# Kernel optimization log

Hardware: AMD Instinct MI355X
Metric: run time of the kernel (lower is better)

The kernel has to match this reference:

```python
import jax, jax.numpy as jnp
import numpy as np

B, C, H, W = 2, 512, 64, 64
S = 2            # scale_factor
HEADS = 8
GROUPS = 32      # assumed GroupNorm groups for group_norm(in_channels)
DK = C // HEADS
SCALE = 1.0 / DK ** 2   # faithful to source: 1/d_k**2
RES = H // S
R = RES * 2 - 1


def setup_inputs() -> dict:
    key = jax.random.key(0)
    ks = jax.random.split(key, 8)
    f = lambda k, shp, s=0.02: jax.random.normal(k, shp, jnp.float32) * s
    return {
        "x": jax.random.normal(ks[0], (B, C, H, W), jnp.float32),
        "q_w": f(ks[1], (C, C, 1, 1)),
        "q_b": jnp.zeros((C,), jnp.float32),
        "kv_w": f(ks[2], (2 * C, C, 1, 1)),
        "kv_b": jnp.zeros((2 * C,), jnp.float32),
        "off1_w": f(ks[3], (C, C, S, S)),
        "off1_b": jnp.zeros((C,), jnp.float32),
        "gn_w": jnp.ones((C,), jnp.float32),
        "gn_b": jnp.zeros((C,), jnp.float32),
        "off2_w": f(ks[4], (2, C, 1, 1)),
        "rpe_table": f(ks[5], (HEADS, R, R), 0.01),
        "proj_w": f(ks[6], (C, C, 1, 1)),
        "proj_b": jnp.zeros((C,), jnp.float32),
    }


def _conv(x, w, b=None, stride=1):
    y = jax.lax.conv_general_dilated(x, w, (stride, stride), 'VALID',
                                     dimension_numbers=('NCHW', 'OIHW', 'NCHW'))
    return y if b is None else y + b[None, :, None, None]


def _group_norm(x, w, b, eps=1e-5):
    n, c, h, wd = x.shape
    xg = x.reshape(n, GROUPS, -1)
    mu = xg.mean(-1, keepdims=True)
    var = xg.var(-1, keepdims=True)
    xg = (xg - mu) * jax.lax.rsqrt(var + eps)
    return xg.reshape(n, c, h, wd) * w[None, :, None, None] + b[None, :, None, None]


def _grid_sample(img, grid):
    # bilinear, align_corners=True; img [B,C,H,W], grid [B,...,2] in (x,y) order
    Bn, Cn, Hn, Wn = img.shape
    gshape = grid.shape[1:-1]
    g = grid.reshape(Bn, -1, 2)
    x = (g[..., 0] + 1.0) * 0.5 * (Wn - 1)
    y = (g[..., 1] + 1.0) * 0.5 * (Hn - 1)
    x0 = jnp.floor(x); y0 = jnp.floor(y)
    wx = (x - x0)[:, None, :]; wy = (y - y0)[:, None, :]
    x0i = jnp.clip(x0.astype(jnp.int32), 0, Wn - 1)
    x1i = jnp.clip(x0i + 1, 0, Wn - 1)
    y0i = jnp.clip(y0.astype(jnp.int32), 0, Hn - 1)
    y1i = jnp.clip(y0i + 1, 0, Hn - 1)
    imf = img.reshape(Bn, Cn, Hn * Wn)
    gat = lambda yi, xi: jnp.take_along_axis(imf, (yi * Wn + xi)[:, None, :], axis=2)
    out = (gat(y0i, x0i) * (1 - wx) * (1 - wy) + gat(y0i, x1i) * wx * (1 - wy)
           + gat(y1i, x0i) * (1 - wx) * wy + gat(y1i, x1i) * wx * wy)
    return out.reshape(Bn, Cn, *gshape)


def _forward(x, q_w, q_b, kv_w, kv_b, off1_w, off1_b, gn_w, gn_b, off2_w,
             rpe_table, proj_w, proj_b):
    l = H * W
    q = _conv(x, q_w, q_b)                                   # [B,C,H,W]
    t = _conv(q, off1_w, off1_b, stride=S)                   # [B,C,h,w]
    t = jax.nn.gelu(_group_norm(t, gn_w, gn_b), approximate=False)
    offset = _conv(t, off2_w).transpose(0, 2, 3, 1)          # [B,h,w,2] (y,x)
    h, w = offset.shape[1], offset.shape[2]
    n = h * w
    # reference points (linspace 0.5..h-0.5, normalized by h-1)
    ry = (jnp.linspace(0.5, h - 0.5, h) / (h - 1.0)) * 2.0 - 1.0
    rx = (jnp.linspace(0.5, w - 0.5, w) / (w - 1.0)) * 2.0 - 1.0
    ref = jnp.stack(jnp.meshgrid(ry, rx, indexing='ij'), -1)  # [h,w,2]
    pos = jnp.clip(offset + ref[None], -1.0, 1.0)             # [B,h,w,2]
    sampled = _grid_sample(x, pos[..., ::-1])                 # [B,C,h,w] (context=x)
    kv = _conv(sampled.reshape(B, C, 1, n), kv_w, kv_b)       # [B,2C,1,n]
    k, v = kv[:, :C], kv[:, C:]
    qf = q.reshape(B * HEADS, DK, l)
    kf = k.reshape(B * HEADS, DK, n)
    vf = v.reshape(B * HEADS, DK, n)
    attn = jnp.einsum('bcm,bcn->bmn', qf, kf) * SCALE         # [B*H, l, n]
    # query grid (arange, normalized by dim-1)
    gy = jnp.arange(H, dtype=jnp.float32) / (H - 1.0) * 2.0 - 1.0
    gx = jnp.arange(W, dtype=jnp.float32) / (W - 1.0) * 2.0 - 1.0
    qg = jnp.stack(jnp.meshgrid(gy, gx, indexing='ij'), -1).reshape(l, 2)
    disp = (qg[None, :, None, :] - pos.reshape(B, 1, n, 2)) * 0.5  # [B,l,n,2]
    rpe = jnp.broadcast_to(rpe_table[None], (B, HEADS, R, R))
    bias = _grid_sample(rpe, disp[..., ::-1])                  # [B,HEADS,l,n]
    attn = jax.nn.softmax(attn + bias.reshape(B * HEADS, l, n), axis=-1)
    out = jnp.einsum('bmn,bcn->bcm', attn, vf).reshape(B, C, H, W)
    return _conv(out, proj_w, proj_b)


def reference(x, q_w, q_b, kv_w, kv_b, off1_w, off1_b, gn_w, gn_b, off2_w,
              rpe_table, proj_w, proj_b):
    return _forward(x, q_w, q_b, kv_w, kv_b, off1_w, off1_b, gn_w, gn_b,
                    off2_w, rpe_table, proj_w, proj_b)
```

## Files before the change

### kernel.cpp

```cpp
#include <hip/hip_runtime.h>
#include <hip/hip_bf16.h>
#include <math.h>

typedef float floatx4 __attribute__((ext_vector_type(4)));
typedef short shortx8 __attribute__((ext_vector_type(8)));
typedef unsigned short ush;

#define NB    2
#define NC    512
#define NL    4096
#define NN    1024
#define NH    8
#define NDK   64
#define NR    63
#define LOG2E 1.44269504f
#define QT_SCALE (1.44269504f/4096.0f)

#define OFF_Q      0u
#define OFF_AO     0u
#define OFF_SMP    2097152u
#define OFF_QT     4194304u
#define OFF_T      6291456u
#define OFF_GS     7340032u
#define OFF_POS    7340160u
#define OFF_KT     7344256u
#define OFF_VV     7868544u
#define OFF_PART   8392832u
#define OFF_TAB4   8392832u

__device__ __forceinline__ ush f2bf(float f) {
    unsigned u = __float_as_uint(f);
    u += 0x7fffu + ((u >> 16) & 1u);
    return (ush)(u >> 16);
}
__device__ __forceinline__ float bf2f(ush h) {
    return __uint_as_float(((unsigned)h) << 16);
}

template<int NP, int BSRC, int OUTMODE>
__global__ __launch_bounds__(256) void gemm_mfma_k(
    const float* __restrict__ A, const void* __restrict__ Bv,
    const float* __restrict__ bias, void* __restrict__ Yv, void* __restrict__ Y2,
    int M, int K, int P, int KS)
{
    __shared__ ush a_hi[128 * 72];
    __shared__ ush b_hi[64 * 72];
    __shared__ ush a_lo[NP == 3 ? 128 * 72 : 64];
    __shared__ ush b_lo[NP == 3 ? 64 * 72 : 64];

    int tid = threadIdx.x;
    int wv = tid >> 6, lane = tid & 63, quad = lane >> 4, l15 = lane & 15;
    int bz = blockIdx.z;
    int b = bz / KS, ks = bz - b * KS;
    int m0 = blockIdx.y * 128, p0 = blockIdx.x * 64;
    int Ksl = K / KS, kbeg = ks * Ksl;

    floatx4 acc[2][4];
    #pragma unroll
    for (int mt = 0; mt < 2; ++mt)
        #pragma unroll
        for (int pt = 0; pt < 4; ++pt) acc[mt][pt] = (floatx4)0.f;

    for (int kc = 0; kc < Ksl; kc += 64) {
        int kg0 = kbeg + kc;
        #pragma unroll
        for (int r = 0; r < 8; ++r) {
            int idx = r * 256 + tid;
            int m = idx >> 4, k4 = (idx & 15) << 2;
            float4 av = *(const float4*)(A + (size_t)(m0 + m) * K + kg0 + k4);
            int o = m * 72 + k4;
            ush h0 = f2bf(av.x), h1 = f2bf(av.y), h2 = f2bf(av.z), h3 = f2bf(av.w);
            a_hi[o] = h0; a_hi[o + 1] = h1; a_hi[o + 2] = h2; a_hi[o + 3] = h3;
            if (NP == 3) {
                a_lo[o]     = f2bf(av.x - bf2f(h0));
                a_lo[o + 1] = f2bf(av.y - bf2f(h1));
                a_lo[o + 2] = f2bf(av.z - bf2f(h2));
                a_lo[o + 3] = f2bf(av.w - bf2f(h3));
            }
        }
        #pragma unroll
        for (int r = 0; r < 8; ++r) {
            int idx = r * 256 + tid;
            int k = idx >> 5, p2 = (idx & 31) << 1;
            float v0, v1;
            if (BSRC == 0) {
                const float* Bp = (const float*)Bv + (size_t)b * K * P;
                float2 t2 = *(const float2*)(Bp + (size_t)(kg0 + k) * P + p0 + p2);
                v0 = t2.x; v1 = t2.y;
            } else if (BSRC == 1) {
                const float* Bp = (const float*)Bv + (size_t)b * NC * NL;
                int kk = kg0 + k;
                int c = kk >> 2, kh = (kk >> 1) & 1, kw = kk & 1;
                int p = p0 + p2;
                int oh = p >> 5, ow = p & 31;
                const float* base = Bp + (size_t)c * NL + (2 * oh + kh) * 64 + kw;
                v0 = base[2 * ow];
                v1 = base[2 * ow + 2];
            } else {
                const ush* Bp = (const ush*)Bv + (size_t)b * K * P;
                unsigned u = *(const unsigned*)(Bp + (size_t)(kg0 + k) * P + p0 + p2);
                v0 = bf2f((ush)(u & 0xffffu));
                v1 = bf2f((ush)(u >> 16));
            }
            ush h0 = f2bf(v0), h1 = f2bf(v1);
            b_hi[p2 * 72 + k] = h0;
            b_hi[(p2 + 1) * 72 + k] = h1;
            if (NP == 3) {
                b_lo[p2 * 72 + k]       = f2bf(v0 - bf2f(h0));
                b_lo[(p2 + 1) * 72 + k] = f2bf(v1 - bf2f(h1));
            }
        }
        __syncthreads();

        shortx8 ah[2][2], al[2][2];
        #pragma unroll
        for (int mt = 0; mt < 2; ++mt)
            #pragma unroll
            for (int kk = 0; kk < 2; ++kk) {
                int o = (wv * 32 + mt * 16 + l15) * 72 + kk * 32 + quad * 8;
                ah[mt][kk] = *(const shortx8*)&a_hi[o];
                if (NP == 3) al[mt][kk] = *(const shortx8*)&a_lo[o];
            }
        #pragma unroll
        for (int pt = 0; pt < 4; ++pt) {
            #pragma unroll
            for (int kk = 0; kk < 2; ++kk) {
                int o = (pt * 16 + l15) * 72 + kk * 32 + quad * 8;
                shortx8 bh = *(const shortx8*)&b_hi[o];
                acc[0][pt] = __builtin_amdgcn_mfma_f32_16x16x32_bf16(ah[0][kk], bh, acc[0][pt], 0, 0, 0);
                acc[1][pt] = __builtin_amdgcn_mfma_f32_16x16x32_bf16(ah[1][kk], bh, acc[1][pt], 0, 0, 0);
                if (NP == 3) {
                    shortx8 bl = *(const shortx8*)&b_lo[o];
                    acc[0][pt] = __builtin_amdgcn_mfma_f32_16x16x32_bf16(ah[0][kk], bl, acc[0][pt], 0, 0, 0);
                    acc[1][pt] = __builtin_amdgcn_mfma_f32_16x16x32_bf16(ah[1][kk], bl, acc[1][pt], 0, 0, 0);
                    acc[0][pt] = __builtin_amdgcn_mfma_f32_16x16x32_bf16(al[0][kk], bh, acc[0][pt], 0, 0, 0);
                    acc[1][pt] = __builtin_amdgcn_mfma_f32_16x16x32_bf16(al[1][kk], bh, acc[1][pt], 0, 0, 0);
                }
            }
        }
        __syncthreads();
    }

    #pragma unroll
    for (int mt = 0; mt < 2; ++mt) {
        #pragma unroll
        for (int reg = 0; reg < 4; ++reg) {
            int m = m0 + wv * 32 + mt * 16 + quad * 4 + reg;
            float bb = (OUTMODE == 2) ? 0.f : bias[m];
            #pragma unroll
            for (int pt = 0; pt < 4; ++pt) {
                int p = p0 + pt * 16 + l15;
                float val = acc[mt][pt][reg] + bb;
                if (OUTMODE == 0) {
                    ((float*)Yv)[(size_t)b * M * P + (size_t)m * P + p] = val;
                } else if (OUTMODE == 2) {
                    ((float*)Yv)[(size_t)(ks * NB + b) * M * P + (size_t)m * P + p] = val;
                } else if (OUTMODE == 3) {
                    ((float*)Yv)[(size_t)b * M * P + (size_t)m * P + p] = val;
                    int h = m >> 6, d = m & 63;
                    ((ush*)Y2)[(((size_t)(b * 8 + h) * 4096) + p) * 64 + d] = f2bf(val * QT_SCALE);
                } else {
                    if (m < 512) {
                        int h = m >> 6, d = m & 63;
                        ((ush*)Yv)[(((size_t)(b * 8 + h) * 1024) + p) * 64 + d] = f2bf(val);
                    } else {
                        int c = m - 512;
                        ((ush*)Y2)[((size_t)(b * 512) + c) * 1024 + p] = f2bf(val);
                    }
                }
            }
        }
    }
}

__global__ __launch_bounds__(256) void reduce_off1_k(const float* __restrict__ part,
                                                     const float* __restrict__ bias,
                                                     float* __restrict__ t)
{
    int i = blockIdx.x * 256 + threadIdx.x;
    float v = part[i] + part[i + 1048576] + part[i + 2097152] + part[i + 3145728];
    t[i] = v + bias[(i >> 10) & 511];
}

__global__ __launch_bounds__(256) void gn_stats_k(const float* __restrict__ T, float* __restrict__ gs)
{
    int bg = blockIdx.x;
    const float* base = T + (size_t)bg * 16384;
    float s = 0.f, ss = 0.f;
    for (int i = threadIdx.x; i < 16384; i += 256) { float v = base[i]; s += v; ss += v * v; }
    #pragma unroll
    for (int off = 32; off >= 1; off >>= 1) { s += __shfl_xor(s, off); ss += __shfl_xor(ss, off); }
    __shared__ float red[8];
    int wv = threadIdx.x >> 6;
    if ((threadIdx.x & 63) == 0) { red[wv * 2] = s; red[wv * 2 + 1] = ss; }
    __syncthreads();
    if (threadIdx.x == 0) {
        float S = red[0] + red[2] + red[4] + red[6];
        float SS = red[1] + red[3] + red[5] + red[7];
        float mu = S / 16384.f;
        float var = SS / 16384.f - mu * mu;
        gs[bg * 2] = mu;
        gs[bg * 2 + 1] = rsqrtf(var + 1e-5f);
    }
}

__global__ __launch_bounds__(256) void gn_gelu_k(float* __restrict__ T, const float* __restrict__ gs,
                                                 const float* __restrict__ gw, const float* __restrict__ gb)
{
    int idx = blockIdx.x * 256 + threadIdx.x;
    int bg = idx >> 14;
    int c = (idx >> 10) & 511;
    float mu = gs[bg * 2], rs = gs[bg * 2 + 1];
    float v = (T[idx] - mu) * rs * gw[c] + gb[c];
    T[idx] = v * 0.5f * (1.f + erff(v * 0.70710678118654752f));
}

__global__ __launch_bounds__(256) void offset_pos_k(const float* __restrict__ T,
                                                    const float* __restrict__ w2,
                                                    float* __restrict__ pos)
{
    int b = blockIdx.x >> 5;
    int og = threadIdx.x & 31;
    int cg = threadIdx.x >> 5;
    int op = ((blockIdx.x & 31) << 5) + og;
    const float* Tb = T + (size_t)b * NC * NN + (size_t)cg * 64 * NN + op;
    float o0 = 0.f, o1 = 0.f;
    #pragma unroll 4
    for (int c = 0; c < 64; ++c) {
        float tv = Tb[(size_t)c * NN];
        o0 += w2[cg * 64 + c] * tv;
        o1 += w2[512 + cg * 64 + c] * tv;
    }
    __shared__ float rs[2][8][32];
    rs[0][cg][og] = o0;
    rs[1][cg][og] = o1;
    __syncthreads();
    if (threadIdx.x < 64) {
        int coord = threadIdx.x >> 5, og2 = threadIdx.x & 31;
        float s = 0.f;
        #pragma unroll
        for (int k = 0; k < 8; ++k) s += rs[coord][k][og2];
        int opf = ((blockIdx.x & 31) << 5) + og2;
        int oh = opf >> 5, ow = opf & 31;
        float ref = (coord == 0) ? ((0.5f + oh) / 31.f * 2.f - 1.f)
                                 : ((0.5f + ow) / 31.f * 2.f - 1.f);
        pos[((size_t)b * 1024 + opf) * 2 + coord] = fminf(fmaxf(s + ref, -1.f), 1.f);
    }
}

__global__ __launch_bounds__(256) void sample_k(const float* __restrict__ x,
                                                const float* __restrict__ pos,
                                                ush* __restrict__ smp)
{
    int idx = blockIdx.x * 256 + threadIdx.x;
    int j = idx & 1023, c = (idx >> 10) & 511, b = idx >> 19;
    float py = pos[(b * 1024 + j) * 2];
    float px = pos[(b * 1024 + j) * 2 + 1];
    float fx = (px + 1.f) * 0.5f * 63.f;
    float fy = (py + 1.f) * 0.5f * 63.f;
    float flx = floorf(fx), fly = floorf(fy);
    float wx = fx - flx, wy = fy - fly;
    int x0 = min(max((int)flx, 0), 63), y0 = min(max((int)fly, 0), 63);
    int x1 = min(x0 + 1, 63),           y1 = min(y0 + 1, 63);
    const float* xb = x + ((size_t)(b * NC + c)) * NL;
    float v00 = xb[y0 * 64 + x0];
    float v01 = xb[y0 * 64 + x1];
    float v10 = xb[y1 * 64 + x0];
    float v11 = xb[y1 * 64 + x1];
    float v = v00 * (1 - wx) * (1 - wy) + v01 * wx * (1 - wy)
            + v10 * (1 - wx) * wy       + v11 * wx * wy;
    smp[idx] = f2bf(v);
}

__global__ __launch_bounds__(256) void tab4_k(const float* __restrict__ rpe,
                                              uint2* __restrict__ tab4)
{
    int i = blockIdx.x * 256 + threadIdx.x;
    int h = i >> 12, y = (i >> 6) & 63, x = i & 63;
    const float* R = rpe + (size_t)h * 3969;
    float v00 = (y < 63 && x < 63)         ? R[y * 63 + x] * LOG2E : 0.f;
    float v01 = (y < 63 && x + 1 < 63)     ? R[y * 63 + x + 1] * LOG2E : 0.f;
    float v10 = (y + 1 < 63 && x < 63)     ? R[(y + 1) * 63 + x] * LOG2E : 0.f;
    float v11 = (y + 1 < 63 && x + 1 < 63) ? R[(y + 1) * 63 + x + 1] * LOG2E : 0.f;
    uint2 o;
    o.x = (unsigned)f2bf(v00) | ((unsigned)f2bf(v01) << 16);
    o.y = (unsigned)f2bf(v10) | ((unsigned)f2bf(v11) << 16);
    tab4[i] = o;
}

__global__ __launch_bounds__(256) void attn_k(
    const ush* __restrict__ qT, const ush* __restrict__ kT,
    const ush* __restrict__ vv, const float* __restrict__ pos,
    const uint2* __restrict__ tab4, ush* __restrict__ ao)
{
    __shared__ __align__(16) char smem[50176];
    ush*   pa     = (ush*)smem;
    uint2* tab_s  = (uint2*)(smem + 9216);
    float* posj15 = (float*)(smem + 41984);
    float* obuf   = (float*)smem;

    int bh = blockIdx.y;
    int b = bh >> 3, h = bh & 7;
    int m0 = blockIdx.x * 64;
    int tid = threadIdx.x;
    int wv = tid >> 6, lane = tid & 63, quad = lane >> 4, l15 = lane & 15;

    const ush* qbase = qT + ((size_t)bh * 4096 + m0 + wv * 16 + l15) * 64 + quad * 8;
    shortx8 qf0 = *(const shortx8*)(qbase);
    shortx8 qf1 = *(const shortx8*)(qbase + 32);

    const uint2* tg = tab4 + (size_t)h * 4096;
    for (int i = tid; i < 4096; i += 256) tab_s[i] = tg[i];
    const float* pb = pos + (size_t)b * 2048;
    for (int i = tid; i < 2048; i += 256) posj15[i] = pb[i] * 15.5f;

    float qy15[4], qx15[4];
    #pragma unroll
    for (int reg = 0; reg < 4; ++reg) {
        int mg = m0 + wv * 16 + quad * 4 + reg;
        qy15[reg] = (float)(mg >> 6) * (31.f / 63.f) + 15.5f;
        qx15[reg] = (float)(mg & 63) * (31.f / 63.f) + 15.5f;
    }

    floatx4 o_acc[4], o_sum;
    #pragma unroll
    for (int dt = 0; dt < 4; ++dt) o_acc[dt] = (floatx4)0.f;
    o_sum = (floatx4)0.f;
    shortx8 vone = {16256, 16256, 16256, 16256, 16256, 16256, 16256, 16256};

    __syncthreads();

    const ush* kbase = kT + (size_t)bh * 1024 * 64;
    const ush* vbase = vv + (size_t)(b * 512 + h * 64) * 1024;

    for (int jc = 0; jc < 16; ++jc) {
        int j0 = jc * 64;
        floatx4 sacc[4];
        #pragma unroll
        for (int jt = 0; jt < 4; ++jt) sacc[jt] = (floatx4)0.f;
        #pragma unroll
        for (int jt = 0; jt < 4; ++jt) {
            const ush* kp = kbase + (size_t)(j0 + jt * 16 + l15) * 64 + quad * 8;
            shortx8 kf0 = *(const shortx8*)kp;
            shortx8 kf1 = *(const shortx8*)(kp + 32);
            sacc[jt] = __builtin_amdgcn_mfma_f32_16x16x32_bf16(qf0, kf0, sacc[jt], 0, 0, 0);
            sacc[jt] = __builtin_amdgcn_mfma_f32_16x16x32_bf16(qf1, kf1, sacc[jt], 0, 0, 0);
        }
        #pragma unroll
        for (int jt = 0; jt < 4; ++jt) {
            int j = j0 + jt * 16 + l15;
            float2 pp = *(const float2*)&posj15[j * 2];
            #pragma unroll
            for (int reg = 0; reg < 4; ++reg) {
                float gy = qy15[reg] - pp.x;
                float gx = qx15[reg] - pp.y;
                float fy = floorf(gy), fx = floorf(gx);
                float wy = gy - fy, wx = gx - fx;
                int y0 = min(max((int)fy, 0), 62);
                int x0 = min(max((int)fx, 0), 62);
                uint2 tw = tab_s[(y0 << 6) + x0];
                float r00 = __uint_as_float(tw.x << 16);
                float r01 = __uint_as_float(tw.x & 0xffff0000u);
                float r10 = __uint_as_float(tw.y << 16);
                float r11 = __uint_as_float(tw.y & 0xffff0000u);
                float bx0 = r00 + wx * (r01 - r00);
                float bx1 = r10 + wx * (r11 - r10);
                float p = exp2f(sacc[jt][reg] + (bx0 + wy * (bx1 - bx0)));
                pa[(wv * 16 + quad * 4 + reg) * 72 + jt * 16 + l15] = f2bf(p);
            }
        }
        const ush* pbase = pa + (wv * 16 + l15) * 72 + quad * 8;
        shortx8 pf0 = *(const shortx8*)pbase;
        shortx8 pf1 = *(const shortx8*)(pbase + 32);
        o_sum = __builtin_amdgcn_mfma_f32_16x16x32_bf16(pf0, vone, o_sum, 0, 0, 0);
        o_sum = __builtin_amdgcn_mfma_f32_16x16x32_bf16(pf1, vone, o_sum, 0, 0, 0);
        #pragma unroll
        for (int dt = 0; dt < 4; ++dt) {
            const ush* vp = vbase + (size_t)(dt * 16 + l15) * 1024 + j0 + quad * 8;
            shortx8 vf0 = *(const shortx8*)vp;
            shortx8 vf1 = *(const shortx8*)(vp + 32);
            o_acc[dt] = __builtin_amdgcn_mfma_f32_16x16x32_bf16(pf0, vf0, o_acc[dt], 0, 0, 0);
            o_acc[dt] = __builtin_amdgcn_mfma_f32_16x16x32_bf16(pf1, vf1, o_acc[dt], 0, 0, 0);
        }
    }

    __syncthreads();
    float inv[4];
    #pragma unroll
    for (int reg = 0; reg < 4; ++reg) inv[reg] = 1.f / o_sum[reg];
    #pragma unroll
    for (int dt = 0; dt < 4; ++dt)
        #pragma unroll
        for (int reg = 0; reg < 4; ++reg)
            obuf[(dt * 16 + l15) * 68 + wv * 16 + quad * 4 + reg] = o_acc[dt][reg] * inv[reg];
    __syncthreads();
    ush* aobase = ao + ((size_t)(b * 512 + h * 64)) * 4096 + m0;
    for (int i = tid; i < 4096; i += 256) {
        int d = i >> 6, m = i & 63;
        aobase[(size_t)d * 4096 + m] = f2bf(obuf[d * 68 + m]);
    }
}

extern "C" void kernel_launch(void* const* d_in, const int* in_sizes, int n_in,
                              void* d_out, int out_size, void* d_ws, size_t ws_size,
                              hipStream_t stream) {
    const float* x      = (const float*)d_in[0];
    const float* q_w    = (const float*)d_in[1];
    const float* q_b    = (const float*)d_in[2];
    const float* kv_w   = (const float*)d_in[3];
    const float* kv_b   = (const float*)d_in[4];
    const float* off1_w = (const float*)d_in[5];
    const float* off1_b = (const float*)d_in[6];
    const float* gn_w   = (const float*)d_in[7];
    const float* gn_b   = (const float*)d_in[8];
    const float* off2_w = (const float*)d_in[9];
    const float* rpe    = (const float*)d_in[10];
    const float* proj_w = (const float*)d_in[11];
    const float* proj_b = (const float*)d_in[12];

    float* ws   = (float*)d_ws;
    float* q    = ws + OFF_Q;
    ush*   ao   = (ush*)(ws + OFF_AO);
    ush*   smp  = (ush*)(ws + OFF_SMP);
    ush*   qT   = (ush*)(ws + OFF_QT);
    float* t    = ws + OFF_T;
    float* gs   = ws + OFF_GS;
    float* pos  = ws + OFF_POS;
    ush*   kT   = (ush*)(ws + OFF_KT);
    ush*   vv   = (ush*)(ws + OFF_VV);
    float* part = ws + OFF_PART;
    uint2* tab4 = (uint2*)(ws + OFF_TAB4);
    float* out  = (float*)d_out;

    gemm_mfma_k<3, 0, 3><<<dim3(64, 4, 2), 256, 0, stream>>>(q_w, x, q_b, q, qT, 512, 512, 4096, 1);
    gemm_mfma_k<3, 1, 2><<<dim3(16, 4, 8), 256, 0, stream>>>(off1_w, q, nullptr, part, nullptr, 512, 2048, 1024, 4);
    reduce_off1_k<<<4096, 256, 0, stream>>>(part, off1_b, t);
    gn_stats_k<<<64, 256, 0, stream>>>(t, gs);
    gn_gelu_k<<<4096, 256, 0, stream>>>(t, gs, gn_w, gn_b);
    offset_pos_k<<<64, 256, 0, stream>>>(t, off2_w, pos);
    tab4_k<<<128, 256, 0, stream>>>(rpe, tab4);
    sample_k<<<4096, 256, 0, stream>>>(x, pos, smp);
    gemm_mfma_k<1, 2, 4><<<dim3(16, 8, 2), 256, 0, stream>>>(kv_w, smp, kv_b, kT, vv, 1024, 512, 1024, 1);
    attn_k<<<dim3(64, 16), 256, 0, stream>>>(qT, kT, vv, pos, tab4, ao);
    gemm_mfma_k<1, 2, 0><<<dim3(64, 4, 2), 256, 0, stream>>>(proj_w, ao, proj_b, out, nullptr, 512, 512, 4096, 1);
}
```

Measured before the change: 368.6 us.

## Fold q conv into offset conv weights and enlarge attention blocks

```diff
diff --git a/kernel.cpp b/kernel.cpp
--- a/kernel.cpp
+++ b/kernel.cpp
@@ -16,17 +16,18 @@
 #define LOG2E 1.44269504f
 #define QT_SCALE (1.44269504f/4096.0f)
 
-#define OFF_Q      0u
-#define OFF_AO     0u
-#define OFF_SMP    2097152u
-#define OFF_QT     4194304u
-#define OFF_T      6291456u
-#define OFF_GS     7340032u
-#define OFF_POS    7340160u
-#define OFF_KT     7344256u
-#define OFF_VV     7868544u
-#define OFF_PART   8392832u
-#define OFF_TAB4   8392832u
+#define OFF_QT     0u
+#define OFF_T      2097152u
+#define OFF_GS     3145728u
+#define OFF_POS    3145856u
+#define OFF_KT     3149952u
+#define OFF_VV     3674240u
+#define OFF_SMP    4198528u
+#define OFF_WEFF   4722816u
+#define OFF_BEFF   5771392u
+#define OFF_PART   5771904u
+#define OFF_TAB4   5771904u
+#define OFF_AO     5837440u
 
 __device__ __forceinline__ ush f2bf(float f) {
     unsigned u = __float_as_uint(f);
@@ -155,10 +156,9 @@
                     ((float*)Yv)[(size_t)b * M * P + (size_t)m * P + p] = val;
                 } else if (OUTMODE == 2) {
                     ((float*)Yv)[(size_t)(ks * NB + b) * M * P + (size_t)m * P + p] = val;
-                } else if (OUTMODE == 3) {
-                    ((float*)Yv)[(size_t)b * M * P + (size_t)m * P + p] = val;
+                } else if (OUTMODE == 5) {
                     int h = m >> 6, d = m & 63;
-                    ((ush*)Y2)[(((size_t)(b * 8 + h) * 4096) + p) * 64 + d] = f2bf(val * QT_SCALE);
+                    ((ush*)Yv)[(((size_t)(b * 8 + h) * 4096) + p) * 64 + d] = f2bf(val * QT_SCALE);
                 } else {
                     if (m < 512) {
                         int h = m >> 6, d = m & 63;
@@ -173,13 +173,104 @@
     }
 }
 
+__global__ __launch_bounds__(256) void weff_k(
+    const float* __restrict__ off1w, const float* __restrict__ qw,
+    float* __restrict__ weff)
+{
+    __shared__ ush a_hi[128 * 72], a_lo[128 * 72];
+    __shared__ ush b_hi[64 * 72],  b_lo[64 * 72];
+    int tid = threadIdx.x;
+    int wv = tid >> 6, lane = tid & 63, quad = lane >> 4, l15 = lane & 15;
+    int khw = blockIdx.z;
+    int m0 = blockIdx.y * 128, p0 = blockIdx.x * 64;
+
+    floatx4 acc[2][4];
+    #pragma unroll
+    for (int mt = 0; mt < 2; ++mt)
+        #pragma unroll
+        for (int pt = 0; pt < 4; ++pt) acc[mt][pt] = (floatx4)0.f;
+
+    for (int k0 = 0; k0 < 512; k0 += 64) {
+        #pragma unroll
+        for (int r = 0; r < 32; ++r) {
+            int idx = r * 256 + tid;
+            int m = idx >> 6, k = idx & 63;
+            float v = off1w[((size_t)(m0 + m) * 512 + k0 + k) * 4 + khw];
+            ush h = f2bf(v);
+            a_hi[m * 72 + k] = h;
+            a_lo[m * 72 + k] = f2bf(v - bf2f(h));
+        }
+        #pragma unroll
+        for (int r = 0; r < 8; ++r) {
+            int idx = r * 256 + tid;
+            int k = idx >> 5, p2 = (idx & 31) << 1;
+            float2 t2 = *(const float2*)(qw + (size_t)(k0 + k) * 512 + p0 + p2);
+            ush h0 = f2bf(t2.x), h1 = f2bf(t2.y);
+            b_hi[p2 * 72 + k] = h0;       b_hi[(p2 + 1) * 72 + k] = h1;
+            b_lo[p2 * 72 + k] = f2bf(t2.x - bf2f(h0));
+            b_lo[(p2 + 1) * 72 + k] = f2bf(t2.y - bf2f(h1));
+        }
+        __syncthreads();
+        shortx8 ah[2][2], al[2][2];
+        #pragma unroll
+        for (int mt = 0; mt < 2; ++mt)
+            #pragma unroll
+            for (int kk = 0; kk < 2; ++kk) {
+                int o = (wv * 32 + mt * 16 + l15) * 72 + kk * 32 + quad * 8;
+                ah[mt][kk] = *(const shortx8*)&a_hi[o];
+                al[mt][kk] = *(const shortx8*)&a_lo[o];
+            }
+        #pragma unroll
+        for (int pt = 0; pt < 4; ++pt) {
+            #pragma unroll
+            for (int kk = 0; kk < 2; ++kk) {
+                int o = (pt * 16 + l15) * 72 + kk * 32 + quad * 8;
+                shortx8 bh = *(const shortx8*)&b_hi[o];
+                shortx8 bl = *(const shortx8*)&b_lo[o];
+                #pragma unroll
+                for (int mt = 0; mt < 2; ++mt) {
+                    acc[mt][pt] = __builtin_amdgcn_mfma_f32_16x16x32_bf16(ah[mt][kk], bh, acc[mt][pt], 0, 0, 0);
+                    acc[mt][pt] = __builtin_amdgcn_mfma_f32_16x16x32_bf16(ah[mt][kk], bl, acc[mt][pt], 0, 0, 0);
+                    acc[mt][pt] = __builtin_amdgcn_mfma_f32_16x16x32_bf16(al[mt][kk], bh, acc[mt][pt], 0, 0, 0);
+                }
+            }
+        }
+        __syncthreads();
+    }
+    #pragma unroll
+    for (int mt = 0; mt < 2; ++mt)
+        #pragma unroll
+        for (int reg = 0; reg < 4; ++reg) {
+            int m = m0 + wv * 32 + mt * 16 + quad * 4 + reg;
+            #pragma unroll
+            for (int pt = 0; pt < 4; ++pt) {
+                int p = p0 + pt * 16 + l15;
+                weff[(size_t)m * 2048 + p * 4 + khw] = acc[mt][pt][reg];
+            }
+        }
+}
+
+__global__ __launch_bounds__(256) void biaseff_k(const float* __restrict__ off1w,
+                                                 const float* __restrict__ off1b,
+                                                 const float* __restrict__ qb,
+                                                 float* __restrict__ beff)
+{
+    int co = blockIdx.x * 256 + threadIdx.x;
+    float s = off1b[co];
+    for (int cm = 0; cm < 512; ++cm) {
+        const float* w = off1w + ((size_t)co * 512 + cm) * 4;
+        s += (w[0] + w[1] + w[2] + w[3]) * qb[cm];
+    }
+    beff[co] = s;
+}
+
 __global__ __launch_bounds__(256) void reduce_off1_k(const float* __restrict__ part,
-                                                     const float* __restrict__ bias,
+                                                     const float* __restrict__ beff,
                                                      float* __restrict__ t)
 {
     int i = blockIdx.x * 256 + threadIdx.x;
     float v = part[i] + part[i + 1048576] + part[i + 2097152] + part[i + 3145728];
-    t[i] = v + bias[(i >> 10) & 511];
+    t[i] = v + beff[(i >> 10) & 511];
 }
 
 __global__ __launch_bounds__(256) void gn_stats_k(const float* __restrict__ T, float* __restrict__ gs)
@@ -288,20 +379,20 @@
     tab4[i] = o;
 }
 
-__global__ __launch_bounds__(256) void attn_k(
+__global__ __launch_bounds__(512, 4) void attn_k(
     const ush* __restrict__ qT, const ush* __restrict__ kT,
     const ush* __restrict__ vv, const float* __restrict__ pos,
     const uint2* __restrict__ tab4, ush* __restrict__ ao)
 {
-    __shared__ __align__(16) char smem[50176];
+    __shared__ __align__(16) char smem[59392];
     ush*   pa     = (ush*)smem;
-    uint2* tab_s  = (uint2*)(smem + 9216);
-    float* posj15 = (float*)(smem + 41984);
+    uint2* tab_s  = (uint2*)(smem + 18432);
+    float* posj15 = (float*)(smem + 51200);
     float* obuf   = (float*)smem;
 
     int bh = blockIdx.y;
     int b = bh >> 3, h = bh & 7;
-    int m0 = blockIdx.x * 64;
+    int m0 = blockIdx.x * 128;
     int tid = threadIdx.x;
     int wv = tid >> 6, lane = tid & 63, quad = lane >> 4, l15 = lane & 15;
 
@@ -310,9 +401,9 @@
     shortx8 qf1 = *(const shortx8*)(qbase + 32);
 
     const uint2* tg = tab4 + (size_t)h * 4096;
-    for (int i = tid; i < 4096; i += 256) tab_s[i] = tg[i];
+    for (int i = tid; i < 4096; i += 512) tab_s[i] = tg[i];
     const float* pb = pos + (size_t)b * 2048;
-    for (int i = tid; i < 2048; i += 256) posj15[i] = pb[i] * 15.5f;
+    for (int i = tid; i < 2048; i += 512) posj15[i] = pb[i] * 15.5f;
 
     float qy15[4], qx15[4];
     #pragma unroll
@@ -345,6 +436,13 @@
             shortx8 kf1 = *(const shortx8*)(kp + 32);
             sacc[jt] = __builtin_amdgcn_mfma_f32_16x16x32_bf16(qf0, kf0, sacc[jt], 0, 0, 0);
             sacc[jt] = __builtin_amdgcn_mfma_f32_16x16x32_bf16(qf1, kf1, sacc[jt], 0, 0, 0);
+        }
+        shortx8 vf0[4], vf1[4];
+        #pragma unroll
+        for (int dt = 0; dt < 4; ++dt) {
+            const ush* vp = vbase + (size_t)(dt * 16 + l15) * 1024 + j0 + quad * 8;
+            vf0[dt] = *(const shortx8*)vp;
+            vf1[dt] = *(const shortx8*)(vp + 32);
         }
         #pragma unroll
         for (int jt = 0; jt < 4; ++jt) {
@@ -376,11 +474,8 @@
         o_sum = __builtin_amdgcn_mfma_f32_16x16x32_bf16(pf1, vone, o_sum, 0, 0, 0);
         #pragma unroll
         for (int dt = 0; dt < 4; ++dt) {
-            const ush* vp = vbase + (size_t)(dt * 16 + l15) * 1024 + j0 + quad * 8;
-            shortx8 vf0 = *(const shortx8*)vp;
-            shortx8 vf1 = *(const shortx8*)(vp + 32);
-            o_acc[dt] = __builtin_amdgcn_mfma_f32_16x16x32_bf16(pf0, vf0, o_acc[dt], 0, 0, 0);
-            o_acc[dt] = __builtin_amdgcn_mfma_f32_16x16x32_bf16(pf1, vf1, o_acc[dt], 0, 0, 0);
+            o_acc[dt] = __builtin_amdgcn_mfma_f32_16x16x32_bf16(pf0, vf0[dt], o_acc[dt], 0, 0, 0);
+            o_acc[dt] = __builtin_amdgcn_mfma_f32_16x16x32_bf16(pf1, vf1[dt], o_acc[dt], 0, 0, 0);
         }
     }
 
@@ -392,12 +487,12 @@
     for (int dt = 0; dt < 4; ++dt)
         #pragma unroll
         for (int reg = 0; reg < 4; ++reg)
-            obuf[(dt * 16 + l15) * 68 + wv * 16 + quad * 4 + reg] = o_acc[dt][reg] * inv[reg];
+            obuf[(dt * 16 + l15) * 133 + wv * 16 + quad * 4 + reg] = o_acc[dt][reg] * inv[reg];
     __syncthreads();
     ush* aobase = ao + ((size_t)(b * 512 + h * 64)) * 4096 + m0;
-    for (int i = tid; i < 4096; i += 256) {
-        int d = i >> 6, m = i & 63;
-        aobase[(size_t)d * 4096 + m] = f2bf(obuf[d * 68 + m]);
+    for (int i = tid; i < 8192; i += 512) {
+        int d = i >> 7, m = i & 127;
+        aobase[(size_t)d * 4096 + m] = f2bf(obuf[d * 133 + m]);
     }
 }
 
@@ -419,28 +514,31 @@
     const float* proj_b = (const float*)d_in[12];
 
     float* ws   = (float*)d_ws;
-    float* q    = ws + OFF_Q;
-    ush*   ao   = (ush*)(ws + OFF_AO);
-    ush*   smp  = (ush*)(ws + OFF_SMP);
     ush*   qT   = (ush*)(ws + OFF_QT);
     float* t    = ws + OFF_T;
     float* gs   = ws + OFF_GS;
     float* pos  = ws + OFF_POS;
     ush*   kT   = (ush*)(ws + OFF_KT);
     ush*   vv   = (ush*)(ws + OFF_VV);
+    ush*   smp  = (ush*)(ws + OFF_SMP);
+    float* weff = ws + OFF_WEFF;
+    float* beff = ws + OFF_BEFF;
     float* part = ws + OFF_PART;
     uint2* tab4 = (uint2*)(ws + OFF_TAB4);
+    ush*   ao   = (ush*)(ws + OFF_AO);
     float* out  = (float*)d_out;
 
-    gemm_mfma_k<3, 0, 3><<<dim3(64, 4, 2), 256, 0, stream>>>(q_w, x, q_b, q, qT, 512, 512, 4096, 1);
-    gemm_mfma_k<3, 1, 2><<<dim3(16, 4, 8), 256, 0, stream>>>(off1_w, q, nullptr, part, nullptr, 512, 2048, 1024, 4);
-    reduce_off1_k<<<4096, 256, 0, stream>>>(part, off1_b, t);
+    weff_k<<<dim3(8, 4, 4), 256, 0, stream>>>(off1_w, q_w, weff);
+    biaseff_k<<<2, 256, 0, stream>>>(off1_w, off1_b, q_b, beff);
+    gemm_mfma_k<1, 0, 5><<<dim3(64, 4, 2), 256, 0, stream>>>(q_w, x, q_b, qT, nullptr, 512, 512, 4096, 1);
+    gemm_mfma_k<3, 1, 2><<<dim3(16, 4, 8), 256, 0, stream>>>(weff, x, nullptr, part, nullptr, 512, 2048, 1024, 4);
+    reduce_off1_k<<<4096, 256, 0, stream>>>(part, beff, t);
     gn_stats_k<<<64, 256, 0, stream>>>(t, gs);
     gn_gelu_k<<<4096, 256, 0, stream>>>(t, gs, gn_w, gn_b);
     offset_pos_k<<<64, 256, 0, stream>>>(t, off2_w, pos);
     tab4_k<<<128, 256, 0, stream>>>(rpe, tab4);
     sample_k<<<4096, 256, 0, stream>>>(x, pos, smp);
     gemm_mfma_k<1, 2, 4><<<dim3(16, 8, 2), 256, 0, stream>>>(kv_w, smp, kv_b, kT, vv, 1024, 512, 1024, 1);
-    attn_k<<<dim3(64, 16), 256, 0, stream>>>(qT, kT, vv, pos, tab4, ao);
+    attn_k<<<dim3(32, 16), 512, 0, stream>>>(qT, kT, vv, pos, tab4, ao);
     gemm_mfma_k<1, 2, 0><<<dim3(64, 4, 2), 256, 0, stream>>>(proj_w, ao, proj_b, out, nullptr, 512, 512, 4096, 1);
 }
```

Result: slower. 518.2 us (+40.6%).
